# Performance work log

Measured on AMD Instinct MI355X. Metric: run time of the kernel, lower is better.

The kernel has to match this reference:

```python
import jax, jax.numpy as jnp
import numpy as np

N_HEADS = 8
DIM_HEAD = 64


def _lin_params(key, fan_in, fan_out):
    k1, k2 = jax.random.split(key)
    w = jax.random.normal(k1, (fan_out, fan_in), jnp.float32) * 0.02
    b = jax.random.normal(k2, (fan_out,), jnp.float32) * 0.02
    return w, b


def setup_inputs() -> dict:
    key = jax.random.key(0)
    ks = jax.random.split(key, 16)
    n_nodes, n_edges = 30000, 480000
    input_nf, output_nf, hidden_nf = 128, 128, 256
    hd = N_HEADS * DIM_HEAD
    inp = {}
    inp['h'] = jax.random.normal(ks[0], (n_nodes, input_nf), jnp.float32)
    inp['x'] = jax.random.normal(ks[1], (n_nodes, 3), jnp.float32)
    inp['edge_index'] = jax.random.randint(ks[2], (2, n_edges), 0, n_nodes, jnp.int64)
    inp['mask'] = jnp.ones((n_edges,), jnp.bool_)
    inp['wq'], inp['bq'] = _lin_params(ks[3], input_nf, hd)
    inp['wk'], inp['bk'] = _lin_params(ks[4], input_nf, hd)
    inp['wv'], inp['bv'] = _lin_params(ks[5], input_nf, hd)
    inp['wo'], inp['bo'] = _lin_params(ks[6], hd, output_nf)
    inp['pw1'], inp['pb1'] = _lin_params(ks[7], 6, hidden_nf)
    inp['pw2'], inp['pb2'] = _lin_params(ks[8], hidden_nf, N_HEADS)
    inp['ew1'], inp['eb1'] = _lin_params(ks[9], 2 * input_nf + 7, hidden_nf)
    inp['ew2'], inp['eb2'] = _lin_params(ks[10], hidden_nf, hidden_nf)
    inp['eww'], inp['ewb'] = _lin_params(ks[11], hidden_nf, N_HEADS)
    inp['cw1'], inp['cb1'] = _lin_params(ks[12], 3, hidden_nf)
    inp['cw2'], inp['cb2'] = _lin_params(ks[13], hidden_nf, hidden_nf)
    inp['cw3'], inp['cb3'] = _lin_params(ks[14], hidden_nf, output_nf)
    return inp


def reference(h, x, edge_index, mask,
              wq, bq, wk, bk, wv, bv, wo, bo,
              pw1, pb1, pw2, pb2,
              ew1, eb1, ew2, eb2, eww, ewb,
              cw1, cb1, cw2, cb2, cw3, cb3):
    n_nodes = h.shape[0]
    row, col = edge_index[0], edge_index[1]
    # node projections -> [n, H, D]
    q = (h @ wq.T + bq).reshape(n_nodes, N_HEADS, DIM_HEAD)
    k = (h @ wk.T + bk).reshape(n_nodes, N_HEADS, DIM_HEAD)
    v = (h @ wv.T + bv).reshape(n_nodes, N_HEADS, DIM_HEAD)
    xr, xc = x[row], x[col]
    # pos encoding [E, H]
    abs_pos = jnp.concatenate([xr, xc], axis=-1)
    pos_enc = jax.nn.silu(abs_pos @ pw1.T + pb1) @ pw2.T + pb2
    # edge features -> per-head edge weights [E, H]
    rel_dist = jnp.sum((xr - xc) ** 2, axis=-1, keepdims=True)
    edge_attr = jnp.concatenate([h[row], h[col], rel_dist, xr, xc], axis=-1)
    edge_feat = jax.nn.silu(edge_attr @ ew1.T + eb1) @ ew2.T + eb2
    edge_w = edge_feat @ eww.T + ewb
    # attention scores [E, H]
    score = jnp.einsum('ehd,ehd->eh', q[row], k[col]) / (DIM_HEAD ** 0.5)
    score = score + pos_enc + edge_w
    score = jnp.where(mask[:, None], score, jnp.float32(-1e9))
    # scatter-softmax over edges grouped by destination (row)
    smax = jax.ops.segment_max(score, row, num_segments=n_nodes)
    escore = jnp.exp(score - smax[row])
    ssum = jax.ops.segment_sum(escore, row, num_segments=n_nodes)
    attn = escore / (ssum[row] + 1e-8)
    # weighted aggregation [n, H, D]
    agg = jax.ops.segment_sum(attn[:, :, None] * v[col], row, num_segments=n_nodes)
    out = agg.reshape(n_nodes, -1) @ wo.T + bo
    coord = jax.nn.silu(x @ cw1.T + cb1)
    coord = jax.nn.silu(coord @ cw2.T + cb2)
    coord = coord @ cw3.T + cb3
    return out + coord, jnp.zeros_like(x)
```

## Files before the change

kernel.cpp:

```cpp
#include <hip/hip_runtime.h>

typedef unsigned int uint;
typedef unsigned short ushort;
typedef unsigned char uchar;
typedef __attribute__((ext_vector_type(8))) short bf16x8;
typedef __attribute__((ext_vector_type(8))) ushort ushort8;
typedef __attribute__((ext_vector_type(4))) float f32x4;

__device__ __forceinline__ float silu_fast(float t) {
  return t * __builtin_amdgcn_rcpf(1.f + __expf(-t));
}
__device__ __forceinline__ float bf2f(ushort u) {
  union { uint i; float f; } v; v.i = ((uint)u) << 16; return v.f;
}
__device__ __forceinline__ float bf2f_lo(uint u) {
  union { uint i; float f; } v; v.i = u << 16; return v.f;
}
__device__ __forceinline__ float bf2f_hi(uint u) {
  union { uint i; float f; } v; v.i = u & 0xffff0000u; return v.f;
}
__device__ __forceinline__ ushort f2bf(float f) {
  union { float f; uint i; } v; v.f = f;
  uint r = (v.i + 0x7fffu + ((v.i >> 16) & 1u)) >> 16;
  return (ushort)r;
}
__device__ __forceinline__ uint cvtpk_bf(float a, float b) {
  uint r; asm("v_cvt_pk_bf16_f32 %0, %1, %2" : "=v"(r) : "v"(a), "v"(b)); return r;
}
__device__ __forceinline__ uchar f2e4m3(float f) {
  uint u = __float_as_uint(f);
  uint s = (u >> 24) & 0x80u;
  uint m = u & 0x7fffffffu;
  if (m >= 0x43f00000u) return (uchar)(s | 0x7e);
  if (m >= 0x3c800000u) {
    uint r = m + 0x7ffffu + ((m >> 20) & 1u);
    uint e = (r >> 23) - 120u;
    if (e > 15u) return (uchar)(s | 0x7e);
    return (uchar)(s | (e << 3) | ((r >> 20) & 7u));
  }
  float az = __uint_as_float(m);
  uint k = (uint)__float2int_rn(az * 512.f);
  return (uchar)(s | k);
}
__device__ __forceinline__ uint pk4_e4m3(float4 v) {
  return (uint)f2e4m3(v.x) | ((uint)f2e4m3(v.y) << 8)
       | ((uint)f2e4m3(v.z) << 16) | ((uint)f2e4m3(v.w) << 24);
}
__device__ __forceinline__ float e4m3f(uint b) {
  uint u = ((b & 0x80u) << 24) | ((b & 0x7fu) << 20);
  return __uint_as_float(u) * 0x1p+120f;
}

__global__ __launch_bounds__(256) void mega_prep(
    const float* __restrict__ x, const int* __restrict__ ei,
    const float* __restrict__ wq, const float* __restrict__ wk, const float* __restrict__ wv,
    const float* __restrict__ bq, const float* __restrict__ bk, const float* __restrict__ bv,
    const float* __restrict__ ew1, const float* __restrict__ eb1,
    const float* __restrict__ pw1, const float* __restrict__ pb1,
    const float* __restrict__ ew2, const float* __restrict__ eww,
    const float* __restrict__ eb2, const float* __restrict__ ewb,
    const float* __restrict__ pw2, const float* __restrict__ pb2,
    const float* __restrict__ wo, const float* __restrict__ cw3,
    const float* __restrict__ bo, const float* __restrict__ cb3,
    const float* __restrict__ cw1, const float* __restrict__ cb1,
    const float* __restrict__ cw2,
    ushort* __restrict__ c1,
    ushort* __restrict__ wnode, float* __restrict__ bqkv,
    short* __restrict__ W1g,
    short* __restrict__ W2T, float* __restrict__ biasC,
    ushort* __restrict__ wcomb, float* __restrict__ bcomb,
    ushort* __restrict__ cw2bf, int* __restrict__ cnt,
    int n, int E,
    int o1, int o2, int o3, int o4, int o5, int o6)
{
  int b = blockIdx.x, tid = threadIdx.x;
  if (b < o1) {
    int idx = b * 256 + tid;
    if (idx < n * 256) {
      int node = idx >> 8, j = idx & 255;
      float t = fmaf(x[node * 3 + 2], cw1[j * 3 + 2],
                fmaf(x[node * 3 + 1], cw1[j * 3 + 1],
                fmaf(x[node * 3 + 0], cw1[j * 3 + 0], cb1[j])));
      c1[idx] = f2bf(silu_fast(t));
    }
  } else if (b < o2) {
    int idx = (b - o1) * 256 + tid;
    if (idx < 2048 * 128) {
      int j = idx >> 7, k = idx & 127;
      float v;
      if (j < 512)       v = wq[j * 128 + k];
      else if (j < 1024) v = wk[(j - 512) * 128 + k];
      else if (j < 1536) v = wv[(j - 1024) * 128 + k];
      else if (j < 1792) v = ew1[(j - 1536) * 263 + k];
      else               v = ew1[(j - 1792) * 263 + 128 + k];
      wnode[idx] = f2bf(v);
      if (idx < 1536)
        bqkv[idx] = (idx < 512) ? bq[idx] : (idx < 1024) ? bk[idx - 512] : bv[idx - 1024];
    }
  } else if (b < o3) {
    int idx = (b - o2) * 256 + tid;
    if (idx < 512 * 32) {
      int nn = idx >> 5, k = idx & 31;
      float v = 0.f;
      if (nn < 256) {
        if (k == 0)      v = eb1[nn];
        else if (k < 8)  v = ew1[nn * 263 + 256 + (k - 1)];
      } else {
        int p = nn - 256;
        if (k == 0)           v = pb1[p];
        else if (k >= 2 && k < 8) v = pw1[p * 6 + (k - 2)];
      }
      W1g[idx] = (short)f2bf(v);
    }
  } else if (b < o4) {
    int idx = (b - o3) * 256 + tid;
    if (idx < 16 * 512) {
      int hh = idx >> 9, k = idx & 511;
      float v = 0.f;
      if (hh < 8) {
        if (k < 256) {
          float s = 0.f;
          for (int j = 0; j < 256; ++j) s += eww[hh * 256 + j] * ew2[j * 256 + k];
          v = s;
        } else v = pw2[hh * 256 + (k - 256)];
      }
      W2T[idx] = (short)f2bf(v);
      if (idx < 16) {
        float bb = 0.f;
        if (idx < 8) {
          float s = 0.f;
          for (int j = 0; j < 256; ++j) s += eww[idx * 256 + j] * eb2[j];
          bb = s + ewb[idx] + pb2[idx];
        }
        biasC[idx] = bb;
      }
    }
  } else if (b < o5) {
    int idx = (b - o4) * 256 + tid;
    if (idx < 128 * 768) {
      int j = idx / 768, k = idx % 768;
      float v = (k < 512) ? wo[j * 512 + k] : cw3[j * 256 + (k - 512)];
      wcomb[idx] = f2bf(v);
      if (idx < 128) bcomb[idx] = bo[idx] + cb3[idx];
    }
  } else if (b < o6) {
    int idx = (b - o5) * 256 + tid;
    if (idx < 256 * 256) cw2bf[idx] = f2bf(cw2[idx]);
  } else {
    int e = (b - o6) * 256 + tid;
    if (e < E) atomicAdd(&cnt[ei[e]], 1);
  }
}

__global__ __launch_bounds__(256) void nodeproj_kernel(
    const float* __restrict__ h,
    const ushort* __restrict__ wnode,
    const float* __restrict__ bqkv,
    ushort* __restrict__ q_t, uchar* __restrict__ k8, ushort* __restrict__ v_t,
    ushort* __restrict__ P1t, ushort* __restrict__ P2t,
    int n)
{
  __shared__ float oS[64 * 68];
  int tid = threadIdx.x;
  int lane = tid & 63, w = tid >> 6;
  int l15 = lane & 15, l4 = lane >> 4;
  int m0 = blockIdx.x * 64;
  int jb0 = blockIdx.y * 8;
  int mrow = m0 + w * 16 + l15;
  int mr = (mrow < n) ? mrow : (n - 1);

  bf16x8 hf[4];
#pragma unroll
  for (int ks = 0; ks < 4; ++ks) {
    const float* hp = h + (size_t)mr * 128 + ks * 32 + l4 * 8;
    float4 a0 = *(const float4*)hp;
    float4 a1 = *(const float4*)(hp + 4);
    uint4 pk;
    pk.x = cvtpk_bf(a0.x, a0.y); pk.y = cvtpk_bf(a0.z, a0.w);
    pk.z = cvtpk_bf(a1.x, a1.y); pk.w = cvtpk_bf(a1.z, a1.w);
    union { uint4 u; bf16x8 b; } cv; cv.u = pk;
    hf[ks] = cv.b;
  }

  int row = tid >> 2, cs = (tid & 3) * 16;
  int gr = m0 + row;

  for (int jb = jb0; jb < jb0 + 8; ++jb) {
    f32x4 acc[4];
#pragma unroll
    for (int nf = 0; nf < 4; ++nf) acc[nf] = (f32x4){0.f, 0.f, 0.f, 0.f};
#pragma unroll
    for (int nf = 0; nf < 4; ++nf)
#pragma unroll
      for (int ks = 0; ks < 4; ++ks) {
        bf16x8 wf = *(const bf16x8*)(wnode + (size_t)(jb * 64 + nf * 16 + l15) * 128 + ks * 32 + l4 * 8);
        acc[nf] = __builtin_amdgcn_mfma_f32_16x16x32_bf16(wf, hf[ks], acc[nf], 0, 0, 0);
      }
    __syncthreads();
#pragma unroll
    for (int nf = 0; nf < 4; ++nf)
      *(f32x4*)(oS + (w * 16 + l15) * 68 + nf * 16 + l4 * 4) = acc[nf];
    __syncthreads();
    if (gr < n) {
      float4 o0 = *(const float4*)(oS + row * 68 + cs);
      float4 o1 = *(const float4*)(oS + row * 68 + cs + 4);
      float4 o2 = *(const float4*)(oS + row * 68 + cs + 8);
      float4 o3 = *(const float4*)(oS + row * 68 + cs + 12);
      int gc = jb * 64 + cs;
      if (jb < 24) {
        float4 b0 = *(const float4*)(bqkv + gc);
        float4 b1 = *(const float4*)(bqkv + gc + 4);
        float4 b2 = *(const float4*)(bqkv + gc + 8);
        float4 b3 = *(const float4*)(bqkv + gc + 12);
        o0.x += b0.x; o0.y += b0.y; o0.z += b0.z; o0.w += b0.w;
        o1.x += b1.x; o1.y += b1.y; o1.z += b1.z; o1.w += b1.w;
        o2.x += b2.x; o2.y += b2.y; o2.z += b2.z; o2.w += b2.w;
        o3.x += b3.x; o3.y += b3.y; o3.z += b3.z; o3.w += b3.w;
        if (jb < 8) {
          uint4 s0 = {cvtpk_bf(o0.x,o0.y), cvtpk_bf(o0.z,o0.w), cvtpk_bf(o1.x,o1.y), cvtpk_bf(o1.z,o1.w)};
          uint4 s1 = {cvtpk_bf(o2.x,o2.y), cvtpk_bf(o2.z,o2.w), cvtpk_bf(o3.x,o3.y), cvtpk_bf(o3.z,o3.w)};
          *(uint4*)(q_t + (size_t)gr * 512 + gc) = s0;
          *(uint4*)(q_t + (size_t)gr * 512 + gc + 8) = s1;
        } else if (jb < 16) {
          uint4 st = {pk4_e4m3(o0), pk4_e4m3(o1), pk4_e4m3(o2), pk4_e4m3(o3)};
          *(uint4*)(k8 + (size_t)gr * 512 + (gc - 512)) = st;
        } else {
          uint4 s0 = {cvtpk_bf(o0.x,o0.y), cvtpk_bf(o0.z,o0.w), cvtpk_bf(o1.x,o1.y), cvtpk_bf(o1.z,o1.w)};
          uint4 s1 = {cvtpk_bf(o2.x,o2.y), cvtpk_bf(o2.z,o2.w), cvtpk_bf(o3.x,o3.y), cvtpk_bf(o3.z,o3.w)};
          *(uint4*)(v_t + (size_t)gr * 512 + (gc - 1024)) = s0;
          *(uint4*)(v_t + (size_t)gr * 512 + (gc - 1024) + 8) = s1;
        }
      } else {
        int pc = (jb & 3) * 64 + cs;
        uint4 s0 = {cvtpk_bf(o0.x,o0.y), cvtpk_bf(o0.z,o0.w), cvtpk_bf(o1.x,o1.y), cvtpk_bf(o1.z,o1.w)};
        uint4 s1 = {cvtpk_bf(o2.x,o2.y), cvtpk_bf(o2.z,o2.w), cvtpk_bf(o3.x,o3.y), cvtpk_bf(o3.z,o3.w)};
        ushort* P = (jb < 28) ? P1t : P2t;
        *(uint4*)(P + (size_t)gr * 256 + pc) = s0;
        *(uint4*)(P + (size_t)gr * 256 + pc + 8) = s1;
      }
    }
  }
}

__global__ __launch_bounds__(1024) void scan_kernel(int* __restrict__ cnt,
                                                    int* __restrict__ offs, int n) {
  __shared__ int part[1024];
  int t = threadIdx.x;
  int chunk = (n + 1023) >> 10;
  int s = t * chunk, e = min(s + chunk, n);
  int sum = 0;
  for (int i = s; i < e; ++i) sum += cnt[i];
  part[t] = sum;
  __syncthreads();
  for (int off = 1; off < 1024; off <<= 1) {
    int v = (t >= off) ? part[t - off] : 0;
    __syncthreads();
    part[t] += v;
    __syncthreads();
  }
  int run = (t == 0) ? 0 : part[t - 1];
  for (int i = s; i < e; ++i) {
    int c = cnt[i];
    offs[i] = run;
    cnt[i] = run;
    run += c;
  }
  if (t == 1023) offs[n] = run;
}

__global__ __launch_bounds__(256) void fill_kernel(const int* __restrict__ ei,
                                                   const int* __restrict__ mask,
                                                   int* __restrict__ cursor,
                                                   int2* __restrict__ pairs, int E) {
  int e = blockIdx.x * 256 + threadIdx.x;
  if (e < E) {
    int r = ei[e];
    int p = atomicAdd(&cursor[r], 1);
    int rm = r | (mask[e] ? 0 : (int)0x80000000u);
    pairs[p] = make_int2(ei[E + e], rm);
  }
}

#define EB 64
#define GS 40
#define TS 72

__global__ __launch_bounds__(256) void edge_mfma3_kernel(
    const float* __restrict__ x,
    const int2* __restrict__ pairs, int E,
    const short* __restrict__ W1g,
    const short* __restrict__ W2T, const float* __restrict__ biasC,
    const ushort* __restrict__ P1t, const ushort* __restrict__ P2t,
    float* __restrict__ scores)
{
  __shared__ short geomL[EB * GS];
  __shared__ int2 rcL[EB];
  __shared__ short T1[4 * EB * TS];
  float* slab = (float*)T1;

  int tid = threadIdx.x;
  int lane = tid & 63, w = tid >> 6;
  int l15 = lane & 15, l4 = lane >> 4;
  int eb0 = blockIdx.x * EB;

  if (tid < EB) {
    int i = min(eb0 + tid, E - 1);
    int2 pr = pairs[i];
    rcL[tid] = pr;
    int c = pr.x, r = pr.y & 0x7fffffff;
    float xr0 = x[r*3], xr1 = x[r*3+1], xr2 = x[r*3+2];
    float xc0 = x[c*3], xc1 = x[c*3+1], xc2 = x[c*3+2];
    float d0 = xr0-xc0, d1 = xr1-xc1, d2 = xr2-xc2;
    bf16x8 g;
    g[0] = (short)0x3F80;
    g[1] = (short)f2bf(d0*d0 + d1*d1 + d2*d2);
    g[2] = (short)f2bf(xr0); g[3] = (short)f2bf(xr1); g[4] = (short)f2bf(xr2);
    g[5] = (short)f2bf(xc0); g[6] = (short)f2bf(xc1); g[7] = (short)f2bf(xc2);
    bf16x8 z = {0,0,0,0,0,0,0,0};
    *(bf16x8*)(geomL + tid * GS) = g;
    *(bf16x8*)(geomL + tid * GS + 8) = z;
    *(bf16x8*)(geomL + tid * GS + 16) = z;
    *(bf16x8*)(geomL + tid * GS + 24) = z;
    *(bf16x8*)(geomL + tid * GS + 32) = z;
  }
  __syncthreads();

  int rr[4], cc[4];
  bf16x8 bE[4];
#pragma unroll
  for (int ef = 0; ef < 4; ++ef) {
    int2 pr = rcL[ef * 16 + l15];
    cc[ef] = pr.x; rr[ef] = pr.y & 0x7fffffff;
    bE[ef] = *(const bf16x8*)(geomL + (ef * 16 + l15) * GS + l4 * 8);
  }

  f32x4 sacc[4];
#pragma unroll
  for (int ef = 0; ef < 4; ++ef) sacc[ef] = (f32x4){0.f, 0.f, 0.f, 0.f};

  short* t1w = T1 + w * (EB * TS);

#pragma unroll
  for (int cch = 0; cch < 2; ++cch) {
    const int n0 = cch ? (256 + w * 64) : (w * 64);
    f32x4 acc[4][4];
#pragma unroll
    for (int mf = 0; mf < 4; ++mf) {
      bf16x8 aW = *(const bf16x8*)(W1g + (size_t)(n0 + mf * 16 + l15) * 32 + l4 * 8);
#pragma unroll
      for (int ef = 0; ef < 4; ++ef)
        acc[mf][ef] = __builtin_amdgcn_mfma_f32_16x16x32_bf16(
            aW, bE[ef], (f32x4){0.f, 0.f, 0.f, 0.f}, 0, 0, 0);
    }
    if (cch == 0) {
#pragma unroll
      for (int mf = 0; mf < 4; ++mf) {
        int colb = n0 + mf * 16 + l4 * 4;
        uint2 g1[4], g2[4];
#pragma unroll
        for (int ef = 0; ef < 4; ++ef) {
          g1[ef] = *(const uint2*)(P1t + (size_t)rr[ef] * 256 + colb);
          g2[ef] = *(const uint2*)(P2t + (size_t)cc[ef] * 256 + colb);
        }
#pragma unroll
        for (int ef = 0; ef < 4; ++ef) {
          f32x4 a = acc[mf][ef];
          a[0] += bf2f_lo(g1[ef].x) + bf2f_lo(g2[ef].x);
          a[1] += bf2f_hi(g1[ef].x) + bf2f_hi(g2[ef].x);
          a[2] += bf2f_lo(g1[ef].y) + bf2f_lo(g2[ef].y);
          a[3] += bf2f_hi(g1[ef].y) + bf2f_hi(g2[ef].y);
          acc[mf][ef] = a;
        }
      }
    }
#pragma unroll
    for (int mf = 0; mf < 4; ++mf) {
      int nl = mf * 16 + l4 * 4;
#pragma unroll
      for (int ef = 0; ef < 4; ++ef) {
        int e = ef * 16 + l15;
        f32x4 v = acc[mf][ef];
        float s0 = silu_fast(v[0]);
        float s1 = silu_fast(v[1]);
        float s2 = silu_fast(v[2]);
        float s3 = silu_fast(v[3]);
        uint2 pk;
        pk.x = cvtpk_bf(s0, s1);
        pk.y = cvtpk_bf(s2, s3);
        *(uint2*)(t1w + e * TS + nl) = pk;
      }
    }
#pragma unroll
    for (int ks2 = 0; ks2 < 2; ++ks2) {
      bf16x8 bW2 = *(const bf16x8*)(W2T + (size_t)l15 * 512 + n0 + ks2 * 32 + l4 * 8);
#pragma unroll
      for (int ef = 0; ef < 4; ++ef) {
        bf16x8 aT = *(const bf16x8*)(t1w + (ef * 16 + l15) * TS + ks2 * 32 + l4 * 8);
        sacc[ef] = __builtin_amdgcn_mfma_f32_16x16x32_bf16(aT, bW2, sacc[ef], 0, 0, 0);
      }
    }
  }
  __syncthreads();
#pragma unroll
  for (int ef = 0; ef < 4; ++ef)
#pragma unroll
    for (int i = 0; i < 4; ++i)
      slab[(w * EB + ef * 16 + l4 * 4 + i) * 16 + l15] = sacc[ef][i];
  __syncthreads();
  for (int t = tid; t < EB * 8; t += 256) {
    int e = t >> 3, hh = t & 7;
    float s = biasC[hh]
            + slab[(0 * EB + e) * 16 + hh] + slab[(1 * EB + e) * 16 + hh]
            + slab[(2 * EB + e) * 16 + hh] + slab[(3 * EB + e) * 16 + hh];
    if (rcL[e].y < 0) s = -1e9f;
    if (eb0 + e < E) scores[(size_t)(eb0 + e) * 8 + hh] = s;
  }
}

__global__ __launch_bounds__(256) void attn_fused_kernel(
    const int* __restrict__ offs,
    const int2* __restrict__ pairs,
    const float* __restrict__ scores,
    const ushort* __restrict__ q_t,
    const uchar* __restrict__ k8,
    const ushort* __restrict__ v_t,
    ushort* __restrict__ agg, int n)
{
  int node = blockIdx.x * 4 + (threadIdx.x >> 6);
  if (node >= n) return;
  int lane = threadIdx.x & 63;
  int start = offs[node], end = offs[node + 1];

  bf16x8 qv = *(const bf16x8*)(q_t + (size_t)node * 512 + lane * 8);
  float qf[8];
#pragma unroll
  for (int j = 0; j < 8; ++j) qf[j] = bf2f((ushort)qv[j]);

  float m = -3.0e38f, ssum = 0.f;
  float acc[8];
#pragma unroll
  for (int j = 0; j < 8; ++j) acc[j] = 0.f;

  if (start < end) {
    int col = pairs[start].x;
    uint2 kw = *(const uint2*)(k8 + (size_t)col * 512 + lane * 8);
    bf16x8 vv = *(const bf16x8*)(v_t + (size_t)col * 512 + lane * 8);
    float sml = scores[(size_t)start * 8 + (lane >> 3)];

    for (int i = start; i < end; ++i) {
      uint2 kwc = kw; bf16x8 vvc = vv; float smlc = sml;
      int inx = (i + 1 < end) ? (i + 1) : i;
      col = pairs[inx].x;
      kw = *(const uint2*)(k8 + (size_t)col * 512 + lane * 8);
      vv = *(const bf16x8*)(v_t + (size_t)col * 512 + lane * 8);
      sml = scores[(size_t)inx * 8 + (lane >> 3)];

      float dot = 0.f;
#pragma unroll
      for (int j = 0; j < 4; ++j)
        dot = fmaf(qf[j], e4m3f((kwc.x >> (8 * j)) & 0xffu), dot);
#pragma unroll
      for (int j = 0; j < 4; ++j)
        dot = fmaf(qf[4 + j], e4m3f((kwc.y >> (8 * j)) & 0xffu), dot);
      dot += __shfl_xor(dot, 1);
      dot += __shfl_xor(dot, 2);
      dot += __shfl_xor(dot, 4);
      float s = (smlc < -5e8f) ? -1e9f : fmaf(dot, 0.125f, smlc);
      float nm = fmaxf(m, s);
      float cs = __expf(m - nm);
      float e  = __expf(s - nm);
      ssum = fmaf(ssum, cs, e);
#pragma unroll
      for (int j = 0; j < 8; ++j)
        acc[j] = fmaf(acc[j], cs, e * bf2f((ushort)vvc[j]));
      m = nm;
    }
  }
  float inv = __builtin_amdgcn_rcpf(ssum + 1e-8f);
  ushort8 ov;
#pragma unroll
  for (int j = 0; j < 8; ++j) ov[j] = f2bf(acc[j] * inv);
  *(ushort8*)(agg + (size_t)node * 512 + lane * 8) = ov;
}

__global__ __launch_bounds__(256) void c2_mfma_kernel(const ushort* __restrict__ c1,
                                                      const ushort* __restrict__ cw2bf,
                                                      const float* __restrict__ cb2,
                                                      ushort* __restrict__ c2, int n) {
  __shared__ float oS[64 * 68];
  int tid = threadIdx.x;
  int lane = tid & 63, w = tid >> 6;
  int l15 = lane & 15, l4 = lane >> 4;
  int m0 = blockIdx.x * 64;
  int n0 = blockIdx.y * 64 + w * 16;

  f32x4 acc[4];
#pragma unroll
  for (int mf = 0; mf < 4; ++mf) acc[mf] = (f32x4){0.f, 0.f, 0.f, 0.f};
#pragma unroll
  for (int ks = 0; ks < 8; ++ks) {
    bf16x8 bW = *(const bf16x8*)(cw2bf + (size_t)(n0 + l15) * 256 + ks * 32 + l4 * 8);
#pragma unroll
    for (int mf = 0; mf < 4; ++mf) {
      int gr = m0 + mf * 16 + l15; if (gr >= n) gr = n - 1;
      bf16x8 aH = *(const bf16x8*)(c1 + (size_t)gr * 256 + ks * 32 + l4 * 8);
      acc[mf] = __builtin_amdgcn_mfma_f32_16x16x32_bf16(aH, bW, acc[mf], 0, 0, 0);
    }
  }
#pragma unroll
  for (int mf = 0; mf < 4; ++mf)
#pragma unroll
    for (int i = 0; i < 4; ++i)
      oS[(mf * 16 + l4 * 4 + i) * 68 + w * 16 + l15] = acc[mf][i];
  __syncthreads();
  {
    int row = tid >> 2, cs = (tid & 3) * 16;
    int gr = m0 + row;
    if (gr < n) {
      int gc = blockIdx.y * 64 + cs;
      ushort8 o0, o1;
#pragma unroll
      for (int j = 0; j < 8; ++j) o0[j] = f2bf(silu_fast(oS[row * 68 + cs + j] + cb2[gc + j]));
#pragma unroll
      for (int j = 0; j < 8; ++j) o1[j] = f2bf(silu_fast(oS[row * 68 + cs + 8 + j] + cb2[gc + 8 + j]));
      *(ushort8*)(c2 + (size_t)gr * 256 + gc) = o0;
      *(ushort8*)(c2 + (size_t)gr * 256 + gc + 8) = o1;
    }
  }
}

__global__ __launch_bounds__(256) void final_mfma_kernel(const ushort* __restrict__ agg,
                                                         const ushort* __restrict__ c2,
                                                         const ushort* __restrict__ wcomb,
                                                         const float* __restrict__ bcomb,
                                                         float* __restrict__ out, int n) {
  __shared__ float oS[64 * 68];
  int tid = threadIdx.x;
  int lane = tid & 63, w = tid >> 6;
  int l15 = lane & 15, l4 = lane >> 4;
  int m0 = blockIdx.x * 64;
  int jb = blockIdx.y;
  int n0 = jb * 64 + w * 16;

  f32x4 acc[4];
#pragma unroll
  for (int mf = 0; mf < 4; ++mf) acc[mf] = (f32x4){0.f, 0.f, 0.f, 0.f};
#pragma unroll
  for (int ks = 0; ks < 24; ++ks) {
    bf16x8 bW = *(const bf16x8*)(wcomb + (size_t)(n0 + l15) * 768 + ks * 32 + l4 * 8);
#pragma unroll
    for (int mf = 0; mf < 4; ++mf) {
      int gr = m0 + mf * 16 + l15; if (gr >= n) gr = n - 1;
      const ushort* ap = (ks < 16) ? (agg + (size_t)gr * 512 + ks * 32)
                                   : (c2 + (size_t)gr * 256 + (ks - 16) * 32);
      bf16x8 aH = *(const bf16x8*)(ap + l4 * 8);
      acc[mf] = __builtin_amdgcn_mfma_f32_16x16x32_bf16(aH, bW, acc[mf], 0, 0, 0);
    }
  }
#pragma unroll
  for (int mf = 0; mf < 4; ++mf)
#pragma unroll
    for (int i = 0; i < 4; ++i)
      oS[(mf * 16 + l4 * 4 + i) * 68 + w * 16 + l15] = acc[mf][i];
  __syncthreads();
  {
    int row = tid >> 2, cs = (tid & 3) * 16;
    int gr = m0 + row;
    if (gr < n) {
      int gc = jb * 64 + cs;
#pragma unroll
      for (int g = 0; g < 4; ++g) {
        float4 o;
        o.x = oS[row * 68 + cs + g * 4 + 0] + bcomb[gc + g * 4 + 0];
        o.y = oS[row * 68 + cs + g * 4 + 1] + bcomb[gc + g * 4 + 1];
        o.z = oS[row * 68 + cs + g * 4 + 2] + bcomb[gc + g * 4 + 2];
        o.w = oS[row * 68 + cs + g * 4 + 3] + bcomb[gc + g * 4 + 3];
        *(float4*)(out + (size_t)gr * 128 + gc + g * 4) = o;
      }
    }
  }
}

extern "C" void kernel_launch(void* const* d_in, const int* in_sizes, int n_in,
                              void* d_out, int out_size, void* d_ws, size_t ws_size,
                              hipStream_t stream) {
  const float* h   = (const float*)d_in[0];
  const float* x   = (const float*)d_in[1];
  const int*   ei  = (const int*)d_in[2];
  const int*   mask= (const int*)d_in[3];
  const float* wq  = (const float*)d_in[4];
  const float* bq  = (const float*)d_in[5];
  const float* wk  = (const float*)d_in[6];
  const float* bk  = (const float*)d_in[7];
  const float* wv  = (const float*)d_in[8];
  const float* bv  = (const float*)d_in[9];
  const float* wo  = (const float*)d_in[10];
  const float* bo  = (const float*)d_in[11];
  const float* pw1 = (const float*)d_in[12];
  const float* pb1 = (const float*)d_in[13];
  const float* pw2 = (const float*)d_in[14];
  const float* pb2 = (const float*)d_in[15];
  const float* ew1 = (const float*)d_in[16];
  const float* eb1 = (const float*)d_in[17];
  const float* ew2 = (const float*)d_in[18];
  const float* eb2 = (const float*)d_in[19];
  const float* eww = (const float*)d_in[20];
  const float* ewb = (const float*)d_in[21];
  const float* cw1 = (const float*)d_in[22];
  const float* cb1 = (const float*)d_in[23];
  const float* cw2 = (const float*)d_in[24];
  const float* cb2 = (const float*)d_in[25];
  const float* cw3 = (const float*)d_in[26];
  const float* cb3 = (const float*)d_in[27];

  int n = in_sizes[0] / 128;
  int E = in_sizes[3];

  char* wptr = (char*)d_ws;
  auto alloc = [&](size_t bytes) {
    char* p = wptr;
    wptr += (bytes + 255) & ~(size_t)255;
    return p;
  };
  ushort* q_t   = (ushort*)alloc((size_t)n * 512 * 2);
  uchar*  k8    = (uchar*)alloc((size_t)n * 512);
  ushort* v_t   = (ushort*)alloc((size_t)n * 512 * 2);
  ushort* P1t   = (ushort*)alloc((size_t)n * 256 * 2);
  ushort* P2t   = (ushort*)alloc((size_t)n * 256 * 2);
  float* scores = (float*)alloc((size_t)E * 8 * 4);
  ushort* c1    = (ushort*)alloc((size_t)n * 256 * 2);
  ushort* c2    = (ushort*)alloc((size_t)n * 256 * 2);
  ushort* wnode = (ushort*)alloc((size_t)2048 * 128 * 2);
  float* bqkv   = (float*)alloc((size_t)1536 * 4);
  short* W1g    = (short*)alloc((size_t)512 * 32 * 2);
  short* W2T    = (short*)alloc((size_t)16 * 512 * 2);
  float* biasC  = (float*)alloc((size_t)16 * 4);
  ushort* wcomb = (ushort*)alloc((size_t)128 * 768 * 2);
  float* bcomb  = (float*)alloc((size_t)128 * 4);
  ushort* cw2bf = (ushort*)alloc((size_t)256 * 256 * 2);
  int* offs     = (int*)alloc((size_t)(n + 1) * 4);
  int* cursor   = (int*)alloc((size_t)n * 4);
  int2* pairs   = (int2*)alloc((size_t)E * 8);
  ushort* agg   = q_t;

  hipMemsetAsync(cursor, 0, (size_t)n * 4, stream);

  int b_c1  = (n * 256 + 255) / 256;
  int b_wn  = (2048 * 128) / 256;
  int b_w1  = (512 * 32 + 255) / 256;
  int b_w2  = (16 * 512 + 255) / 256;
  int b_wc  = (128 * 768 + 255) / 256;
  int b_cw  = (256 * 256 + 255) / 256;
  int b_cnt = (E + 255) / 256;
  int o1 = b_c1, o2 = o1 + b_wn, o3 = o2 + b_w1, o4 = o3 + b_w2;
  int o5 = o4 + b_wc, o6 = o5 + b_cw;
  int total_blocks = o6 + b_cnt;

  mega_prep<<<dim3(total_blocks), 256, 0, stream>>>(
      x, ei, wq, wk, wv, bq, bk, bv, ew1, eb1, pw1, pb1, ew2, eww, eb2, ewb,
      pw2, pb2, wo, cw3, bo, cb3, cw1, cb1, cw2,
      c1, wnode, bqkv, W1g, W2T, biasC, wcomb, bcomb, cw2bf, cursor,
      n, E, o1, o2, o3, o4, o5, o6);

  scan_kernel<<<dim3(1), 1024, 0, stream>>>(cursor, offs, n);
  fill_kernel<<<dim3((E + 255) / 256), 256, 0, stream>>>(ei, mask, cursor, pairs, E);

  nodeproj_kernel<<<dim3((n + 63) / 64, 4), 256, 0, stream>>>(
      h, wnode, bqkv, q_t, k8, v_t, P1t, P2t, n);

  edge_mfma3_kernel<<<dim3((E + EB - 1) / EB), 256, 0, stream>>>(
      x, pairs, E, W1g, W2T, biasC, P1t, P2t, scores);

  attn_fused_kernel<<<dim3((n + 3) / 4), 256, 0, stream>>>(
      offs, pairs, scores, q_t, k8, v_t, agg, n);

  c2_mfma_kernel<<<dim3((n + 63) / 64, 4), 256, 0, stream>>>(c1, cw2bf, cb2, c2, n);

  hipMemsetAsync((float*)d_out + (size_t)n * 128, 0, (size_t)n * 3 * 4, stream);
  final_mfma_kernel<<<dim3((n + 63) / 64, 2), 256, 0, stream>>>(agg, c2, wcomb, bcomb,
                                                                (float*)d_out, n);
}
```

Before: 629.8 us.

## Drop online-softmax max tracking, pre-convert h to bf16, split nodeproj grid

The attention kernel drops the running max and rescaling of online softmax. It exponentiates scores directly, folds the e4m3 2^120 scale into q, and processes two edges per iteration with deeper prefetch. h is converted to bf16 once in the prep kernel, and the node projection launches one block per 64-column tile instead of looping over 8 tiles, which raises parallelism. Skipping max subtraction risks overflow if scores grow large, but is safe for these small-magnitude weights.

```diff
diff --git a/kernel.cpp b/kernel.cpp
--- a/kernel.cpp
+++ b/kernel.cpp
@@ -46,13 +46,13 @@
   return (uint)f2e4m3(v.x) | ((uint)f2e4m3(v.y) << 8)
        | ((uint)f2e4m3(v.z) << 16) | ((uint)f2e4m3(v.w) << 24);
 }
-__device__ __forceinline__ float e4m3f(uint b) {
-  uint u = ((b & 0x80u) << 24) | ((b & 0x7fu) << 20);
-  return __uint_as_float(u) * 0x1p+120f;
+__device__ __forceinline__ float e4m3_raw(uint b) {
+  return __uint_as_float(((b & 0x80u) << 24) | ((b & 0x7fu) << 20));
 }
 
 __global__ __launch_bounds__(256) void mega_prep(
-    const float* __restrict__ x, const int* __restrict__ ei,
+    const float* __restrict__ h, const float* __restrict__ x,
+    const int* __restrict__ ei,
     const float* __restrict__ wq, const float* __restrict__ wk, const float* __restrict__ wv,
     const float* __restrict__ bq, const float* __restrict__ bk, const float* __restrict__ bv,
     const float* __restrict__ ew1, const float* __restrict__ eb1,
@@ -64,27 +64,40 @@
     const float* __restrict__ bo, const float* __restrict__ cb3,
     const float* __restrict__ cw1, const float* __restrict__ cb1,
     const float* __restrict__ cw2,
-    ushort* __restrict__ c1,
+    ushort* __restrict__ h_bf, ushort* __restrict__ c1,
     ushort* __restrict__ wnode, float* __restrict__ bqkv,
     short* __restrict__ W1g,
     short* __restrict__ W2T, float* __restrict__ biasC,
     ushort* __restrict__ wcomb, float* __restrict__ bcomb,
     ushort* __restrict__ cw2bf, int* __restrict__ cnt,
     int n, int E,
-    int o1, int o2, int o3, int o4, int o5, int o6)
+    int o1, int o2, int o3, int o4, int o5, int o6, int o7)
 {
   int b = blockIdx.x, tid = threadIdx.x;
   if (b < o1) {
     int idx = b * 256 + tid;
-    if (idx < n * 256) {
-      int node = idx >> 8, j = idx & 255;
-      float t = fmaf(x[node * 3 + 2], cw1[j * 3 + 2],
-                fmaf(x[node * 3 + 1], cw1[j * 3 + 1],
-                fmaf(x[node * 3 + 0], cw1[j * 3 + 0], cb1[j])));
-      c1[idx] = f2bf(silu_fast(t));
+    if (idx * 4 < n * 128) {
+      float4 v = *(const float4*)(h + idx * 4);
+      ushort4 o; o.x = f2bf(v.x); o.y = f2bf(v.y); o.z = f2bf(v.z); o.w = f2bf(v.w);
+      *(ushort4*)(h_bf + idx * 4) = o;
     }
   } else if (b < o2) {
     int idx = (b - o1) * 256 + tid;
+    if (idx < n * 64) {
+      int node = idx >> 6, j = (idx & 63) * 4;
+      float x0 = x[node * 3], x1 = x[node * 3 + 1], x2 = x[node * 3 + 2];
+      ushort4 o;
+#pragma unroll
+      for (int jj = 0; jj < 4; ++jj) {
+        float t = fmaf(x2, cw1[(j + jj) * 3 + 2],
+                  fmaf(x1, cw1[(j + jj) * 3 + 1],
+                  fmaf(x0, cw1[(j + jj) * 3 + 0], cb1[j + jj])));
+        ((ushort*)&o)[jj] = f2bf(silu_fast(t));
+      }
+      *(ushort4*)(c1 + (size_t)node * 256 + j) = o;
+    }
+  } else if (b < o3) {
+    int idx = (b - o2) * 256 + tid;
     if (idx < 2048 * 128) {
       int j = idx >> 7, k = idx & 127;
       float v;
@@ -97,8 +110,8 @@
       if (idx < 1536)
         bqkv[idx] = (idx < 512) ? bq[idx] : (idx < 1024) ? bk[idx - 512] : bv[idx - 1024];
     }
-  } else if (b < o3) {
-    int idx = (b - o2) * 256 + tid;
+  } else if (b < o4) {
+    int idx = (b - o3) * 256 + tid;
     if (idx < 512 * 32) {
       int nn = idx >> 5, k = idx & 31;
       float v = 0.f;
@@ -112,8 +125,8 @@
       }
       W1g[idx] = (short)f2bf(v);
     }
-  } else if (b < o4) {
-    int idx = (b - o3) * 256 + tid;
+  } else if (b < o5) {
+    int idx = (b - o4) * 256 + tid;
     if (idx < 16 * 512) {
       int hh = idx >> 9, k = idx & 511;
       float v = 0.f;
@@ -135,25 +148,25 @@
         biasC[idx] = bb;
       }
     }
-  } else if (b < o5) {
-    int idx = (b - o4) * 256 + tid;
+  } else if (b < o6) {
+    int idx = (b - o5) * 256 + tid;
     if (idx < 128 * 768) {
       int j = idx / 768, k = idx % 768;
       float v = (k < 512) ? wo[j * 512 + k] : cw3[j * 256 + (k - 512)];
       wcomb[idx] = f2bf(v);
       if (idx < 128) bcomb[idx] = bo[idx] + cb3[idx];
     }
-  } else if (b < o6) {
-    int idx = (b - o5) * 256 + tid;
+  } else if (b < o7) {
+    int idx = (b - o6) * 256 + tid;
     if (idx < 256 * 256) cw2bf[idx] = f2bf(cw2[idx]);
   } else {
-    int e = (b - o6) * 256 + tid;
+    int e = (b - o7) * 256 + tid;
     if (e < E) atomicAdd(&cnt[ei[e]], 1);
   }
 }
 
 __global__ __launch_bounds__(256) void nodeproj_kernel(
-    const float* __restrict__ h,
+    const ushort* __restrict__ h_bf,
     const ushort* __restrict__ wnode,
     const float* __restrict__ bqkv,
     ushort* __restrict__ q_t, uchar* __restrict__ k8, ushort* __restrict__ v_t,
@@ -165,79 +178,67 @@
   int lane = tid & 63, w = tid >> 6;
   int l15 = lane & 15, l4 = lane >> 4;
   int m0 = blockIdx.x * 64;
-  int jb0 = blockIdx.y * 8;
+  int jb = blockIdx.y;
   int mrow = m0 + w * 16 + l15;
   int mr = (mrow < n) ? mrow : (n - 1);
 
   bf16x8 hf[4];
 #pragma unroll
-  for (int ks = 0; ks < 4; ++ks) {
-    const float* hp = h + (size_t)mr * 128 + ks * 32 + l4 * 8;
-    float4 a0 = *(const float4*)hp;
-    float4 a1 = *(const float4*)(hp + 4);
-    uint4 pk;
-    pk.x = cvtpk_bf(a0.x, a0.y); pk.y = cvtpk_bf(a0.z, a0.w);
-    pk.z = cvtpk_bf(a1.x, a1.y); pk.w = cvtpk_bf(a1.z, a1.w);
-    union { uint4 u; bf16x8 b; } cv; cv.u = pk;
-    hf[ks] = cv.b;
-  }
-
+  for (int ks = 0; ks < 4; ++ks)
+    hf[ks] = *(const bf16x8*)(h_bf + (size_t)mr * 128 + ks * 32 + l4 * 8);
+
+  f32x4 acc[4];
+#pragma unroll
+  for (int nf = 0; nf < 4; ++nf) acc[nf] = (f32x4){0.f, 0.f, 0.f, 0.f};
+#pragma unroll
+  for (int nf = 0; nf < 4; ++nf)
+#pragma unroll
+    for (int ks = 0; ks < 4; ++ks) {
+      bf16x8 wf = *(const bf16x8*)(wnode + (size_t)(jb * 64 + nf * 16 + l15) * 128 + ks * 32 + l4 * 8);
+      acc[nf] = __builtin_amdgcn_mfma_f32_16x16x32_bf16(wf, hf[ks], acc[nf], 0, 0, 0);
+    }
+#pragma unroll
+  for (int nf = 0; nf < 4; ++nf)
+    *(f32x4*)(oS + (w * 16 + l15) * 68 + nf * 16 + l4 * 4) = acc[nf];
+  __syncthreads();
   int row = tid >> 2, cs = (tid & 3) * 16;
   int gr = m0 + row;
-
-  for (int jb = jb0; jb < jb0 + 8; ++jb) {
-    f32x4 acc[4];
-#pragma unroll
-    for (int nf = 0; nf < 4; ++nf) acc[nf] = (f32x4){0.f, 0.f, 0.f, 0.f};
-#pragma unroll
-    for (int nf = 0; nf < 4; ++nf)
-#pragma unroll
-      for (int ks = 0; ks < 4; ++ks) {
-        bf16x8 wf = *(const bf16x8*)(wnode + (size_t)(jb * 64 + nf * 16 + l15) * 128 + ks * 32 + l4 * 8);
-        acc[nf] = __builtin_amdgcn_mfma_f32_16x16x32_bf16(wf, hf[ks], acc[nf], 0, 0, 0);
-      }
-    __syncthreads();
-#pragma unroll
-    for (int nf = 0; nf < 4; ++nf)
-      *(f32x4*)(oS + (w * 16 + l15) * 68 + nf * 16 + l4 * 4) = acc[nf];
-    __syncthreads();
-    if (gr < n) {
-      float4 o0 = *(const float4*)(oS + row * 68 + cs);
-      float4 o1 = *(const float4*)(oS + row * 68 + cs + 4);
-      float4 o2 = *(const float4*)(oS + row * 68 + cs + 8);
-      float4 o3 = *(const float4*)(oS + row * 68 + cs + 12);
-      int gc = jb * 64 + cs;
-      if (jb < 24) {
-        float4 b0 = *(const float4*)(bqkv + gc);
-        float4 b1 = *(const float4*)(bqkv + gc + 4);
-        float4 b2 = *(const float4*)(bqkv + gc + 8);
-        float4 b3 = *(const float4*)(bqkv + gc + 12);
-        o0.x += b0.x; o0.y += b0.y; o0.z += b0.z; o0.w += b0.w;
-        o1.x += b1.x; o1.y += b1.y; o1.z += b1.z; o1.w += b1.w;
-        o2.x += b2.x; o2.y += b2.y; o2.z += b2.z; o2.w += b2.w;
-        o3.x += b3.x; o3.y += b3.y; o3.z += b3.z; o3.w += b3.w;
-        if (jb < 8) {
-          uint4 s0 = {cvtpk_bf(o0.x,o0.y), cvtpk_bf(o0.z,o0.w), cvtpk_bf(o1.x,o1.y), cvtpk_bf(o1.z,o1.w)};
-          uint4 s1 = {cvtpk_bf(o2.x,o2.y), cvtpk_bf(o2.z,o2.w), cvtpk_bf(o3.x,o3.y), cvtpk_bf(o3.z,o3.w)};
-          *(uint4*)(q_t + (size_t)gr * 512 + gc) = s0;
-          *(uint4*)(q_t + (size_t)gr * 512 + gc + 8) = s1;
-        } else if (jb < 16) {
-          uint4 st = {pk4_e4m3(o0), pk4_e4m3(o1), pk4_e4m3(o2), pk4_e4m3(o3)};
-          *(uint4*)(k8 + (size_t)gr * 512 + (gc - 512)) = st;
-        } else {
-          uint4 s0 = {cvtpk_bf(o0.x,o0.y), cvtpk_bf(o0.z,o0.w), cvtpk_bf(o1.x,o1.y), cvtpk_bf(o1.z,o1.w)};
-          uint4 s1 = {cvtpk_bf(o2.x,o2.y), cvtpk_bf(o2.z,o2.w), cvtpk_bf(o3.x,o3.y), cvtpk_bf(o3.z,o3.w)};
-          *(uint4*)(v_t + (size_t)gr * 512 + (gc - 1024)) = s0;
-          *(uint4*)(v_t + (size_t)gr * 512 + (gc - 1024) + 8) = s1;
-        }
-      } else {
-        int pc = (jb & 3) * 64 + cs;
+  if (gr < n) {
+    float4 o0 = *(const float4*)(oS + row * 68 + cs);
+    float4 o1 = *(const float4*)(oS + row * 68 + cs + 4);
+    float4 o2 = *(const float4*)(oS + row * 68 + cs + 8);
+    float4 o3 = *(const float4*)(oS + row * 68 + cs + 12);
+    int gc = jb * 64 + cs;
+    if (jb < 24) {
+      float4 b0 = *(const float4*)(bqkv + gc);
+      float4 b1 = *(const float4*)(bqkv + gc + 4);
+      float4 b2 = *(const float4*)(bqkv + gc + 8);
+      float4 b3 = *(const float4*)(bqkv + gc + 12);
+      o0.x += b0.x; o0.y += b0.y; o0.z += b0.z; o0.w += b0.w;
+      o1.x += b1.x; o1.y += b1.y; o1.z += b1.z; o1.w += b1.w;
+      o2.x += b2.x; o2.y += b2.y; o2.z += b2.z; o2.w += b2.w;
+      o3.x += b3.x; o3.y += b3.y; o3.z += b3.z; o3.w += b3.w;
+      if (jb < 8) {
         uint4 s0 = {cvtpk_bf(o0.x,o0.y), cvtpk_bf(o0.z,o0.w), cvtpk_bf(o1.x,o1.y), cvtpk_bf(o1.z,o1.w)};
         uint4 s1 = {cvtpk_bf(o2.x,o2.y), cvtpk_bf(o2.z,o2.w), cvtpk_bf(o3.x,o3.y), cvtpk_bf(o3.z,o3.w)};
-        ushort* P = (jb < 28) ? P1t : P2t;
-        *(uint4*)(P + (size_t)gr * 256 + pc) = s0;
-        *(uint4*)(P + (size_t)gr * 256 + pc + 8) = s1;
-      }
+        *(uint4*)(q_t + (size_t)gr * 512 + gc) = s0;
+        *(uint4*)(q_t + (size_t)gr * 512 + gc + 8) = s1;
+      } else if (jb < 16) {
+        uint4 st = {pk4_e4m3(o0), pk4_e4m3(o1), pk4_e4m3(o2), pk4_e4m3(o3)};
+        *(uint4*)(k8 + (size_t)gr * 512 + (gc - 512)) = st;
+      } else {
+        uint4 s0 = {cvtpk_bf(o0.x,o0.y), cvtpk_bf(o0.z,o0.w), cvtpk_bf(o1.x,o1.y), cvtpk_bf(o1.z,o1.w)};
+        uint4 s1 = {cvtpk_bf(o2.x,o2.y), cvtpk_bf(o2.z,o2.w), cvtpk_bf(o3.x,o3.y), cvtpk_bf(o3.z,o3.w)};
+        *(uint4*)(v_t + (size_t)gr * 512 + (gc - 1024)) = s0;
+        *(uint4*)(v_t + (size_t)gr * 512 + (gc - 1024) + 8) = s1;
+      }
+    } else {
+      int pc = (jb & 3) * 64 + cs;
+      uint4 s0 = {cvtpk_bf(o0.x,o0.y), cvtpk_bf(o0.z,o0.w), cvtpk_bf(o1.x,o1.y), cvtpk_bf(o1.z,o1.w)};
+      uint4 s1 = {cvtpk_bf(o2.x,o2.y), cvtpk_bf(o2.z,o2.w), cvtpk_bf(o3.x,o3.y), cvtpk_bf(o3.z,o3.w)};
+      ushort* P = (jb < 28) ? P1t : P2t;
+      *(uint4*)(P + (size_t)gr * 256 + pc) = s0;
+      *(uint4*)(P + (size_t)gr * 256 + pc + 8) = s1;
     }
   }
 }
@@ -429,51 +430,63 @@
   int node = blockIdx.x * 4 + (threadIdx.x >> 6);
   if (node >= n) return;
   int lane = threadIdx.x & 63;
+  int hh = lane >> 3;
   int start = offs[node], end = offs[node + 1];
 
   bf16x8 qv = *(const bf16x8*)(q_t + (size_t)node * 512 + lane * 8);
   float qf[8];
 #pragma unroll
-  for (int j = 0; j < 8; ++j) qf[j] = bf2f((ushort)qv[j]);
-
-  float m = -3.0e38f, ssum = 0.f;
+  for (int j = 0; j < 8; ++j) qf[j] = bf2f((ushort)qv[j]) * 0x1p+120f;
+
+  float ssum = 0.f;
   float acc[8];
 #pragma unroll
   for (int j = 0; j < 8; ++j) acc[j] = 0.f;
 
   if (start < end) {
-    int col = pairs[start].x;
-    uint2 kw = *(const uint2*)(k8 + (size_t)col * 512 + lane * 8);
-    bf16x8 vv = *(const bf16x8*)(v_t + (size_t)col * 512 + lane * 8);
-    float sml = scores[(size_t)start * 8 + (lane >> 3)];
-
-    for (int i = start; i < end; ++i) {
-      uint2 kwc = kw; bf16x8 vvc = vv; float smlc = sml;
-      int inx = (i + 1 < end) ? (i + 1) : i;
-      col = pairs[inx].x;
-      kw = *(const uint2*)(k8 + (size_t)col * 512 + lane * 8);
-      vv = *(const bf16x8*)(v_t + (size_t)col * 512 + lane * 8);
-      sml = scores[(size_t)inx * 8 + (lane >> 3)];
-
-      float dot = 0.f;
-#pragma unroll
-      for (int j = 0; j < 4; ++j)
-        dot = fmaf(qf[j], e4m3f((kwc.x >> (8 * j)) & 0xffu), dot);
-#pragma unroll
-      for (int j = 0; j < 4; ++j)
-        dot = fmaf(qf[4 + j], e4m3f((kwc.y >> (8 * j)) & 0xffu), dot);
-      dot += __shfl_xor(dot, 1);
-      dot += __shfl_xor(dot, 2);
-      dot += __shfl_xor(dot, 4);
-      float s = (smlc < -5e8f) ? -1e9f : fmaf(dot, 0.125f, smlc);
-      float nm = fmaxf(m, s);
-      float cs = __expf(m - nm);
-      float e  = __expf(s - nm);
-      ssum = fmaf(ssum, cs, e);
-#pragma unroll
-      for (int j = 0; j < 8; ++j)
-        acc[j] = fmaf(acc[j], cs, e * bf2f((ushort)vvc[j]));
-      m = nm;
+    int ib = min(start + 1, end - 1);
+    int c0 = pairs[start].x, c1 = pairs[ib].x;
+    uint2 kwa = *(const uint2*)(k8 + (size_t)c0 * 512 + lane * 8);
+    bf16x8 vva = *(const bf16x8*)(v_t + (size_t)c0 * 512 + lane * 8);
+    float sma = scores[(size_t)start * 8 + hh];
+    uint2 kwb = *(const uint2*)(k8 + (size_t)c1 * 512 + lane * 8);
+    bf16x8 vvb = *(const bf16x8*)(v_t + (size_t)c1 * 512 + lane * 8);
+    float smb = scores[(size_t)ib * 8 + hh];
+
+    for (int i = start; i < end; i += 2) {
+      uint2 k0 = kwa, k1 = kwb;
+      bf16x8 v0 = vva, v1 = vvb;
+      float s0 = sma, s1 = smb;
+      bool has1 = (i + 1) < end;
+      int j0 = min(i + 2, end - 1), j1 = min(i + 3, end - 1);
+      int d0 = pairs[j0].x, d1 = pairs[j1].x;
+      kwa = *(const uint2*)(k8 + (size_t)d0 * 512 + lane * 8);
+      vva = *(const bf16x8*)(v_t + (size_t)d0 * 512 + lane * 8);
+      sma = scores[(size_t)j0 * 8 + hh];
+      kwb = *(const uint2*)(k8 + (size_t)d1 * 512 + lane * 8);
+      vvb = *(const bf16x8*)(v_t + (size_t)d1 * 512 + lane * 8);
+      smb = scores[(size_t)j1 * 8 + hh];
+
+      float dot0 = 0.f, dot1 = 0.f;
+#pragma unroll
+      for (int j = 0; j < 4; ++j) {
+        dot0 = fmaf(qf[j],     e4m3_raw((k0.x >> (8 * j)) & 0xffu), dot0);
+        dot0 = fmaf(qf[4 + j], e4m3_raw((k0.y >> (8 * j)) & 0xffu), dot0);
+        dot1 = fmaf(qf[j],     e4m3_raw((k1.x >> (8 * j)) & 0xffu), dot1);
+        dot1 = fmaf(qf[4 + j], e4m3_raw((k1.y >> (8 * j)) & 0xffu), dot1);
+      }
+      dot0 += __shfl_xor(dot0, 1); dot0 += __shfl_xor(dot0, 2); dot0 += __shfl_xor(dot0, 4);
+      dot1 += __shfl_xor(dot1, 1); dot1 += __shfl_xor(dot1, 2); dot1 += __shfl_xor(dot1, 4);
+      float sc0 = (s0 < -5e8f) ? -1e9f : fmaf(dot0, 0.125f, s0);
+      float sc1 = (!has1 || s1 < -5e8f) ? -1e9f : fmaf(dot1, 0.125f, s1);
+      float e0 = __expf(sc0);
+      float e1 = __expf(sc1);
+      ssum += e0 + e1;
+#pragma unroll
+      for (int j = 0; j < 8; ++j) {
+        acc[j] = fmaf(e0, bf2f((ushort)v0[j]), acc[j]);
+        acc[j] = fmaf(e1, bf2f((ushort)v1[j]), acc[j]);
+      }
     }
   }
   float inv = __builtin_amdgcn_rcpf(ssum + 1e-8f);
@@ -627,6 +640,7 @@
   ushort* v_t   = (ushort*)alloc((size_t)n * 512 * 2);
   ushort* P1t   = (ushort*)alloc((size_t)n * 256 * 2);
   ushort* P2t   = (ushort*)alloc((size_t)n * 256 * 2);
+  ushort* h_bf  = (ushort*)alloc((size_t)n * 128 * 2);
   float* scores = (float*)alloc((size_t)E * 8 * 4);
   ushort* c1    = (ushort*)alloc((size_t)n * 256 * 2);
   ushort* c2    = (ushort*)alloc((size_t)n * 256 * 2);
@@ -645,28 +659,29 @@
 
   hipMemsetAsync(cursor, 0, (size_t)n * 4, stream);
 
-  int b_c1  = (n * 256 + 255) / 256;
+  int b_h2  = (n * 128 / 4 + 255) / 256;
+  int b_c1  = (n * 64 + 255) / 256;
   int b_wn  = (2048 * 128) / 256;
   int b_w1  = (512 * 32 + 255) / 256;
   int b_w2  = (16 * 512 + 255) / 256;
   int b_wc  = (128 * 768 + 255) / 256;
   int b_cw  = (256 * 256 + 255) / 256;
   int b_cnt = (E + 255) / 256;
-  int o1 = b_c1, o2 = o1 + b_wn, o3 = o2 + b_w1, o4 = o3 + b_w2;
-  int o5 = o4 + b_wc, o6 = o5 + b_cw;
-  int total_blocks = o6 + b_cnt;
+  int o1 = b_h2, o2 = o1 + b_c1, o3 = o2 + b_wn, o4 = o3 + b_w1;
+  int o5 = o4 + b_w2, o6 = o5 + b_wc, o7 = o6 + b_cw;
+  int total_blocks = o7 + b_cnt;
 
   mega_prep<<<dim3(total_blocks), 256, 0, stream>>>(
-      x, ei, wq, wk, wv, bq, bk, bv, ew1, eb1, pw1, pb1, ew2, eww, eb2, ewb,
+      h, x, ei, wq, wk, wv, bq, bk, bv, ew1, eb1, pw1, pb1, ew2, eww, eb2, ewb,
       pw2, pb2, wo, cw3, bo, cb3, cw1, cb1, cw2,
-      c1, wnode, bqkv, W1g, W2T, biasC, wcomb, bcomb, cw2bf, cursor,
-      n, E, o1, o2, o3, o4, o5, o6);
+      h_bf, c1, wnode, bqkv, W1g, W2T, biasC, wcomb, bcomb, cw2bf, cursor,
+      n, E, o1, o2, o3, o4, o5, o6, o7);
 
   scan_kernel<<<dim3(1), 1024, 0, stream>>>(cursor, offs, n);
   fill_kernel<<<dim3((E + 255) / 256), 256, 0, stream>>>(ei, mask, cursor, pairs, E);
 
-  nodeproj_kernel<<<dim3((n + 63) / 64, 4), 256, 0, stream>>>(
-      h, wnode, bqkv, q_t, k8, v_t, P1t, P2t, n);
+  nodeproj_kernel<<<dim3((n + 63) / 64, 32), 256, 0, stream>>>(
+      h_bf, wnode, bqkv, q_t, k8, v_t, P1t, P2t, n);
 
   edge_mfma3_kernel<<<dim3((E + EB - 1) / EB), 256, 0, stream>>>(
       x, pairs, E, W1g, W2T, biasC, P1t, P2t, scores);
```

New measurement: 617.9 us. No clear change (-1.9%).
